# Optimization experiments

Hardware: AMD Instinct MI355X
Metric: run time of the kernel (lower is better)

## Reference

```python
import jax, jax.numpy as jnp
import numpy as np

NUM_HEADS = 16
LAMBDA = 0.1
HADAMARD_SCALE = 0.05
ROPE_BASE = 10000.0


def _rope(t):
    # t: [B, H, S, hd] -- rotary embedding (half-split convention)
    hd = t.shape[-1]
    S = t.shape[2]
    half = hd // 2
    inv_freq = 1.0 / (ROPE_BASE ** (jnp.arange(half, dtype=jnp.float32) / half))
    ang = jnp.arange(S, dtype=jnp.float32)[:, None] * inv_freq[None, :]  # [S, half]
    cos = jnp.cos(ang).astype(t.dtype)
    sin = jnp.sin(ang).astype(t.dtype)
    t1, t2 = t[..., :half], t[..., half:]
    return jnp.concatenate([t1 * cos - t2 * sin, t2 * cos + t1 * sin], axis=-1)


def _rotate_half(t):
    half = t.shape[-1] // 2
    return jnp.concatenate([-t[..., half:], t[..., :half]], axis=-1)


def setup_inputs() -> dict:
    key = jax.random.key(0)
    ks = jax.random.split(key, 6)
    B, S, D = 2, 2048, 1024
    scale = 1.0 / np.sqrt(D).astype(np.float32)
    x = jax.random.normal(ks[0], (B, S, D), jnp.float32)
    Wq = jax.random.normal(ks[1], (D, D), jnp.float32) * scale
    Wk = jax.random.normal(ks[2], (D, D), jnp.float32) * scale
    Wv = jax.random.normal(ks[3], (D, D), jnp.float32) * scale
    Wo = jax.random.normal(ks[4], (D, D), jnp.float32) * scale
    gate_w = jax.random.normal(ks[5], (D // NUM_HEADS,), jnp.float32) * 0.01
    return {"x": x, "Wq": Wq, "Wk": Wk, "Wv": Wv, "Wo": Wo, "gate_w": gate_w}


def reference(x, Wq, Wk, Wv, Wo, gate_w):
    B, S, D = x.shape
    H = NUM_HEADS
    hd = D // H

    def heads(W):
        return (x @ W.T).reshape(B, S, H, hd).transpose(0, 2, 1, 3)  # [B,H,S,hd]

    Q = _rope(heads(Wq))
    K = _rope(heads(Wk))
    V = heads(Wv)

    causal = jnp.tril(jnp.ones((S, S), dtype=bool))
    inv_sqrt_d = 1.0 / jnp.sqrt(jnp.asarray(hd, x.dtype))

    def attend(q, k):
        # first-order + lambda * second-order (elementwise-squared) scores
        s = (jnp.einsum('bhsd,bhtd->bhst', q, k)
             + LAMBDA * jnp.einsum('bhsd,bhtd->bhst', q * q, k * k)) * inv_sqrt_d
        s = jnp.where(causal, s, jnp.asarray(-1e9, s.dtype))
        a = jax.nn.softmax(s, axis=-1)
        return jnp.einsum('bhst,bhtd->bhsd', a, V)

    out1 = attend(Q, K)                                  # standard pass
    out2 = attend(_rotate_half(Q), _rotate_half(K))      # rotated second pass

    # hadamard gate mix of the two passes
    out = 0.5 * (out1 + out2) + HADAMARD_SCALE * (out1 * out2) * gate_w

    out = out.transpose(0, 2, 1, 3).reshape(B, S, D)
    return out @ Wo.T
```

## Files before the change

kernel.cpp:

```cpp
#include <hip/hip_runtime.h>

typedef unsigned short u16;
typedef __attribute__((ext_vector_type(4))) unsigned short u16x4;
typedef __attribute__((ext_vector_type(8))) unsigned short u16x8;
typedef __attribute__((ext_vector_type(8))) short s16x8;
typedef __attribute__((ext_vector_type(4))) float f32x4;

__device__ __forceinline__ u16 f2bf(float f) {
  unsigned int u = __float_as_uint(f);
  u += 0x7FFFu + ((u >> 16) & 1u);
  return (u16)(u >> 16);
}
__device__ __forceinline__ float bf2f(u16 h) {
  return __uint_as_float(((unsigned int)h) << 16);
}

__device__ __forceinline__ void gload_lds16(const u16* g, u16* l) {
  __builtin_amdgcn_global_load_lds(
      (const __attribute__((address_space(1))) unsigned int*)(g),
      (__attribute__((address_space(3))) unsigned int*)(l), 16, 0, 0);
}

__global__ __launch_bounds__(256) void cvt_all(const float* __restrict__ x,
                                               const float* __restrict__ Wq,
                                               const float* __restrict__ Wk,
                                               const float* __restrict__ Wv,
                                               const float* __restrict__ Wo,
                                               u16* __restrict__ xbf,
                                               u16* __restrict__ wbf,
                                               u16* __restrict__ wobf) {
  int blk = blockIdx.x;
  const float* src;
  u16* dst;
  int i;
  if (blk < 4096) {
    src = x; dst = xbf; i = blk * 256 + threadIdx.x;
  } else {
    int wb = blk - 4096;
    int sel = wb >> 10;
    src = (sel == 0) ? Wq : (sel == 1) ? Wk : (sel == 2) ? Wv : Wo;
    dst = (sel < 3) ? (wbf + (size_t)sel * 1048576) : wobf;
    i = (wb & 1023) * 256 + threadIdx.x;
  }
  float4 v = reinterpret_cast<const float4*>(src)[i];
  u16x4 o;
  o.x = f2bf(v.x); o.y = f2bf(v.y); o.z = f2bf(v.z); o.w = f2bf(v.w);
  reinterpret_cast<u16x4*>(dst)[i] = o;
}

__device__ __forceinline__ void store_out(float* p, float v) { *p = v; }
__device__ __forceinline__ void store_out(u16* p, float v) { *p = f2bf(v); }

template <typename OutT, int WM, int WN>
__global__ __launch_bounds__(256) void gemm_bt(const u16* __restrict__ A,
                                               const u16* __restrict__ Bw,
                                               OutT* __restrict__ C, int N, int K) {
  __shared__ u16 As[2][WM * 1024];
  __shared__ u16 Bs[2][WN * 1024];
  const int tid = threadIdx.x;
  const int lane = tid & 63;
  const int wave = tid >> 6;
  const int wm = wave >> 1, wn = wave & 1;
  const int lh = lane & 15, quad = lane >> 4;
  const int q8 = quad * 8;
  const int m0 = blockIdx.y * (WM * 32), n0 = blockIdx.x * (WN * 32);
  constexpr int NCH = 2 * (WM + WN);
  constexpr int PER = NCH / 4;

  auto stage = [&](int buf, int kt) {
    const int kb = kt * 32;
#pragma unroll
    for (int i = 0; i < PER; ++i) {
      const int c = wave * PER + i;
      if (c < 2 * WM) {
        gload_lds16(A + (size_t)(m0 + c * 16 + lh) * K + kb + q8,
                    &As[buf][c * 512 + lane * 8]);
      } else {
        const int rb = c - 2 * WM;
        gload_lds16(Bw + (size_t)(n0 + rb * 16 + lh) * K + kb + q8,
                    &Bs[buf][rb * 512 + lane * 8]);
      }
    }
  };

  f32x4 acc[WM][WN];
#pragma unroll
  for (int i = 0; i < WM; ++i)
#pragma unroll
    for (int j = 0; j < WN; ++j) { acc[i][j][0] = 0.f; acc[i][j][1] = 0.f; acc[i][j][2] = 0.f; acc[i][j][3] = 0.f; }

  const int nkt = K >> 5;
  stage(0, 0);
  __syncthreads();
  for (int kt = 0; kt < nkt; ++kt) {
    const int p = kt & 1;
    if (kt < nkt - 1) stage(1 - p, kt + 1);
    s16x8 af[WM], bf4[WN];
#pragma unroll
    for (int mb = 0; mb < WM; ++mb)
      af[mb] = *reinterpret_cast<const s16x8*>(&As[p][(wm * WM + mb) * 512 + lane * 8]);
#pragma unroll
    for (int nb = 0; nb < WN; ++nb)
      bf4[nb] = *reinterpret_cast<const s16x8*>(&Bs[p][(wn * WN + nb) * 512 + lane * 8]);
#pragma unroll
    for (int mb = 0; mb < WM; ++mb)
#pragma unroll
      for (int nb = 0; nb < WN; ++nb)
        acc[mb][nb] = __builtin_amdgcn_mfma_f32_16x16x32_bf16(af[mb], bf4[nb], acc[mb][nb], 0, 0, 0);
    __syncthreads();
  }
#pragma unroll
  for (int mb = 0; mb < WM; ++mb)
#pragma unroll
    for (int nb = 0; nb < WN; ++nb) {
      const int col = n0 + wn * (WN * 16) + nb * 16 + lh;
#pragma unroll
      for (int r = 0; r < 4; ++r) {
        const int row = m0 + wm * (WM * 16) + mb * 16 + quad * 4 + r;
        store_out(&C[(size_t)row * N + col], acc[mb][nb][r]);
      }
    }
}

__global__ __launch_bounds__(256) void qkv_gemm(const u16* __restrict__ A,
                                                const u16* __restrict__ Bw,
                                                u16* __restrict__ Vt,
                                                u16* __restrict__ Qs,
                                                u16* __restrict__ Kb,
                                                u16* __restrict__ K2b) {
  __shared__ u16 As[2][4096];
  __shared__ u16 Bs[2][4096];
  const int tid = threadIdx.x;
  const int lane = tid & 63;
  const int wave = tid >> 6;
  const int wm = wave >> 1, wn = wave & 1;
  const int lh = lane & 15, quad = lane >> 4;
  const int q8 = quad * 8;
  const int bx = blockIdx.x;
  const int m0 = blockIdx.y * 128, n0 = bx * 128;
  const int K = 1024;

  auto stage = [&](int buf, int kt) {
    const int kb = kt * 32;
#pragma unroll
    for (int i = 0; i < 4; ++i) {
      const int c = wave * 4 + i;
      if (c < 8) {
        gload_lds16(A + (size_t)(m0 + c * 16 + lh) * K + kb + q8,
                    &As[buf][c * 512 + lane * 8]);
      } else {
        const int rb = c - 8;
        gload_lds16(Bw + (size_t)(n0 + rb * 16 + lh) * K + kb + q8,
                    &Bs[buf][rb * 512 + lane * 8]);
      }
    }
  };

  f32x4 acc[4][4];
#pragma unroll
  for (int i = 0; i < 4; ++i)
#pragma unroll
    for (int j = 0; j < 4; ++j) { acc[i][j][0] = 0.f; acc[i][j][1] = 0.f; acc[i][j][2] = 0.f; acc[i][j][3] = 0.f; }

  stage(0, 0);
  __syncthreads();
  for (int kt = 0; kt < 32; ++kt) {
    const int p = kt & 1;
    if (kt < 31) stage(1 - p, kt + 1);
    s16x8 af[4], bf4[4];
#pragma unroll
    for (int mb = 0; mb < 4; ++mb)
      af[mb] = *reinterpret_cast<const s16x8*>(&As[p][(wm * 4 + mb) * 512 + lane * 8]);
#pragma unroll
    for (int nb = 0; nb < 4; ++nb)
      bf4[nb] = *reinterpret_cast<const s16x8*>(&Bs[p][(wn * 4 + nb) * 512 + lane * 8]);
#pragma unroll
    for (int mb = 0; mb < 4; ++mb)
#pragma unroll
      for (int nb = 0; nb < 4; ++nb)
        acc[mb][nb] = __builtin_amdgcn_mfma_f32_16x16x32_bf16(af[mb], bf4[nb], acc[mb][nb], 0, 0, 0);
    __syncthreads();
  }

  if (bx < 16) {
    const bool isQ = (bx < 8);
#pragma unroll
    for (int nb = 0; nb < 2; ++nb) {
      const int d = nb * 16 + lh;
      const float invf = __expf((float)d * -0.2878231366f);
      const int col = n0 + wn * 64 + nb * 16 + lh;
      const int ch = col & 1023;
      const int h = ch >> 6;
#pragma unroll
      for (int mb = 0; mb < 4; ++mb)
#pragma unroll
        for (int r = 0; r < 4; ++r) {
          const int row = m0 + wm * 64 + mb * 16 + quad * 4 + r;
          const int s = row & 2047, b = row >> 11;
          float ang = (float)s * invf;
          float sv, cv;
          __sincosf(ang, &sv, &cv);
          const float v1 = acc[mb][nb][r], v2 = acc[mb][nb + 2][r];
          const float e0 = v1 * cv - v2 * sv;
          const float e1 = v2 * cv + v1 * sv;
          const size_t ofs = (size_t)((b * 16 + h) * 2048 + s) * 64 + d;
          if (isQ) {
            Qs[ofs]      = f2bf(e0 * 0.125f);
            Qs[ofs + 32] = f2bf(e1 * 0.125f);
          } else {
            Kb[ofs]       = f2bf(e0);
            Kb[ofs + 32]  = f2bf(e1);
            K2b[ofs]      = f2bf(e0 * e0);
            K2b[ofs + 32] = f2bf(e1 * e1);
          }
        }
    }
  } else {
#pragma unroll
    for (int mb = 0; mb < 4; ++mb)
#pragma unroll
      for (int nb = 0; nb < 4; ++nb) {
        const int col = n0 + wn * 64 + nb * 16 + lh;
        const int ch = col & 1023;
        const int h = ch >> 6, d = ch & 63;
        const int row0 = m0 + wm * 64 + mb * 16 + quad * 4;
        const int s0 = row0 & 2047, b = row0 >> 11;
        u16x4 o;
#pragma unroll
        for (int r = 0; r < 4; ++r) o[r] = f2bf(acc[mb][nb][r]);
        *reinterpret_cast<u16x4*>(Vt + (size_t)((b * 16 + h) * 64 + d) * 2048 + s0) = o;
      }
  }
}

__global__ __launch_bounds__(256, 2) void attn_kernel(const u16* __restrict__ Qs,
                                                      const u16* __restrict__ Kb,
                                                      const u16* __restrict__ K2b,
                                                      const u16* __restrict__ Vt,
                                                      const float* __restrict__ gate,
                                                      u16* __restrict__ attn,
                                                      float* __restrict__ Opart,
                                                      float* __restrict__ Lpart,
                                                      float* __restrict__ Opart2,
                                                      float* __restrict__ Lpart2) {
  const int lin = blockIdx.y * 44 + blockIdx.x;
  const int xcd = lin & 7;
  const int slot = lin >> 3;
  const int bh = xcd * 4 + (slot / 44);
  const int bxv = slot % 44;

  int qi, kt0, kt1, chunk, which;
  bool split;
  if (bxv < 32) {
    qi = 15 - (bxv >> 2); chunk = bxv & 3; split = true; which = 0;
    const int T = 2 * qi + 2;
    kt0 = (chunk * T) >> 2;
    kt1 = (((chunk + 1) * T) >> 2) - 1;
  } else if (bxv < 40) {
    const int t = bxv - 32;
    qi = 7 - (t >> 1); chunk = t & 1; split = true; which = 1;
    const int nk = qi + 1; kt0 = chunk * nk; kt1 = kt0 + nk - 1;
  } else {
    qi = 43 - bxv; split = false; which = 0; chunk = 0; kt0 = 0; kt1 = 2 * qi + 1;
  }
  const int tid = threadIdx.x, lane = tid & 63, wave = tid >> 6;
  const int lh = lane & 15, quad = lane >> 4;
  const int b = bh >> 4, h = bh & 15;
  __shared__ u16 Pbuf[4][2][1152];
  const int base = qi * 128 + wave * 32;
  const int q8 = quad * 8;

  s16x8 qf[2][2], q2f[2][2];
#pragma unroll
  for (int mb = 0; mb < 2; ++mb) {
    const size_t qoff = (size_t)(bh * 2048 + base + mb * 16 + lh) * 64 + q8;
#pragma unroll
    for (int kk = 0; kk < 2; ++kk) {
      qf[mb][kk] = *reinterpret_cast<const s16x8*>(Qs + qoff + kk * 32);
#pragma unroll
      for (int j = 0; j < 8; ++j) {
        float f = bf2f((u16)qf[mb][kk][j]);
        q2f[mb][kk][j] = (short)f2bf(f * f * 0.8f);
      }
    }
  }

  f32x4 oacc[2][4];
  float lsum[2][4];
#pragma unroll
  for (int mb = 0; mb < 2; ++mb)
#pragma unroll
    for (int nb = 0; nb < 4; ++nb) { oacc[mb][nb][0] = 0.f; oacc[mb][nb][1] = 0.f; oacc[mb][nb][2] = 0.f; oacc[mb][nb][3] = 0.f; }
#pragma unroll
  for (int mb = 0; mb < 2; ++mb)
#pragma unroll
    for (int r = 0; r < 4; ++r) lsum[mb][r] = 0.f;
  float gw[4];
#pragma unroll
  for (int nb = 0; nb < 4; ++nb) gw[nb] = gate[nb * 16 + lh];

  const int wmaxrow = base + 31;
  const int ktdiag = wmaxrow >> 6;
  const int ktw1 = (kt1 < ktdiag) ? kt1 : ktdiag;

  for (int kt = kt0; kt <= ktw1; ++kt) {
    f32x4 sacc[2][4];
#pragma unroll
    for (int mb = 0; mb < 2; ++mb)
#pragma unroll
      for (int nb = 0; nb < 4; ++nb) { sacc[mb][nb][0] = -8.f; sacc[mb][nb][1] = -8.f; sacc[mb][nb][2] = -8.f; sacc[mb][nb][3] = -8.f; }
    __builtin_amdgcn_s_setprio(1);
#pragma unroll
    for (int nb = 0; nb < 4; ++nb) {
      const size_t krow = (size_t)(bh * 2048 + kt * 64 + nb * 16 + lh) * 64 + q8;
#pragma unroll
      for (int kk = 0; kk < 2; ++kk) {
        s16x8 kf  = *reinterpret_cast<const s16x8*>(Kb  + krow + kk * 32);
        s16x8 k2f = *reinterpret_cast<const s16x8*>(K2b + krow + kk * 32);
#pragma unroll
        for (int mb = 0; mb < 2; ++mb) {
          sacc[mb][nb] = __builtin_amdgcn_mfma_f32_16x16x32_bf16(qf[mb][kk],  kf,  sacc[mb][nb], 0, 0, 0);
          sacc[mb][nb] = __builtin_amdgcn_mfma_f32_16x16x32_bf16(q2f[mb][kk], k2f, sacc[mb][nb], 0, 0, 0);
        }
      }
    }
    __builtin_amdgcn_s_setprio(0);
    s16x8 vf[2][4];
#pragma unroll
    for (int kk = 0; kk < 2; ++kk)
#pragma unroll
      for (int nb = 0; nb < 4; ++nb)
        vf[kk][nb] = *reinterpret_cast<const s16x8*>(
            Vt + (size_t)(bh * 64 + nb * 16 + lh) * 2048 + kt * 64 + kk * 32 + q8);

    if (kt * 64 + 63 > base) {
#pragma unroll
      for (int mb = 0; mb < 2; ++mb)
#pragma unroll
        for (int nb = 0; nb < 4; ++nb) {
          const int colg = kt * 64 + nb * 16 + lh;
#pragma unroll
          for (int r = 0; r < 4; ++r) {
            const int rowg = base + mb * 16 + quad * 4 + r;
            if (colg > rowg) sacc[mb][nb][r] = -1e9f;
          }
        }
    }
#pragma unroll
    for (int mb = 0; mb < 2; ++mb)
#pragma unroll
      for (int nb = 0; nb < 4; ++nb)
#pragma unroll
        for (int r = 0; r < 4; ++r) {
          float pv = __expf(sacc[mb][nb][r]);
          lsum[mb][r] += pv;
          Pbuf[wave][mb][(quad * 4 + r) * 72 + nb * 16 + lh] = f2bf(pv);
        }
    __builtin_amdgcn_s_setprio(1);
#pragma unroll
    for (int mb = 0; mb < 2; ++mb)
#pragma unroll
      for (int kk = 0; kk < 2; ++kk) {
        s16x8 pf = *reinterpret_cast<const s16x8*>(&Pbuf[wave][mb][lh * 72 + kk * 32 + q8]);
#pragma unroll
        for (int nb = 0; nb < 4; ++nb)
          oacc[mb][nb] = __builtin_amdgcn_mfma_f32_16x16x32_bf16(pf, vf[kk][nb], oacc[mb][nb], 0, 0, 0);
      }
    __builtin_amdgcn_s_setprio(0);
  }
#pragma unroll
  for (int mb = 0; mb < 2; ++mb)
#pragma unroll
    for (int r = 0; r < 4; ++r) {
      float rs = lsum[mb][r];
#pragma unroll
      for (int off = 1; off < 16; off <<= 1) rs += __shfl_xor(rs, off);
      lsum[mb][r] = rs;
    }
  if (split) {
#pragma unroll
    for (int mb = 0; mb < 2; ++mb)
#pragma unroll
      for (int r = 0; r < 4; ++r) {
        const int rowg = base + mb * 16 + quad * 4 + r;
        if (which == 0) {
          const size_t orow = (size_t)chunk * 32768 + bh * 1024 + (rowg - 1024);
          if (lh == 0) Lpart[orow] = lsum[mb][r];
#pragma unroll
          for (int nb = 0; nb < 4; ++nb)
            Opart[orow * 64 + nb * 16 + lh] = oacc[mb][nb][r];
        } else {
          const size_t orow = (size_t)chunk * 16384 + bh * 512 + (rowg - 512);
          if (lh == 0) Lpart2[orow] = lsum[mb][r];
#pragma unroll
          for (int nb = 0; nb < 4; ++nb)
            Opart2[orow * 64 + nb * 16 + lh] = oacc[mb][nb][r];
        }
      }
  } else {
#pragma unroll
    for (int mb = 0; mb < 2; ++mb)
#pragma unroll
      for (int r = 0; r < 4; ++r) {
        const float invl = 1.0f / lsum[mb][r];
        const int rows = base + mb * 16 + quad * 4 + r;
#pragma unroll
        for (int nb = 0; nb < 4; ++nb) {
          float o = oacc[mb][nb][r] * invl;
          float val = o + 0.05f * o * o * gw[nb];
          attn[(size_t)(b * 2048 + rows) * 1024 + h * 64 + nb * 16 + lh] = f2bf(val);
        }
      }
  }
}

__global__ __launch_bounds__(256) void combine_kernel(const float* __restrict__ Opart,
                                                      const float* __restrict__ Lpart,
                                                      const float* __restrict__ Opart2,
                                                      const float* __restrict__ Lpart2,
                                                      const float* __restrict__ gate,
                                                      u16* __restrict__ attn) {
  int idx = blockIdx.x * 256 + threadIdx.x;
  int d = idx & 63;
  int r_all = idx >> 6;
  float o, l;
  int bh, s;
  if (r_all < 32768) {
    o = Opart[idx] + Opart[idx + 2097152] + Opart[idx + 4194304] + Opart[idx + 6291456];
    l = Lpart[r_all] + Lpart[r_all + 32768] + Lpart[r_all + 65536] + Lpart[r_all + 98304];
    bh = r_all >> 10; s = 1024 + (r_all & 1023);
  } else {
    const int r2 = r_all - 32768;
    const int i2 = idx - 2097152;
    o = Opart2[i2] + Opart2[i2 + 1048576];
    l = Lpart2[r2] + Lpart2[r2 + 16384];
    bh = r2 >> 9; s = 512 + (r2 & 511);
  }
  o /= l;
  float val = o + 0.05f * o * o * gate[d];
  int b = bh >> 4, h = bh & 15;
  attn[(size_t)(b * 2048 + s) * 1024 + h * 64 + d] = f2bf(val);
}

extern "C" void kernel_launch(void* const* d_in, const int* in_sizes, int n_in,
                              void* d_out, int out_size, void* d_ws, size_t ws_size,
                              hipStream_t stream) {
  (void)in_sizes; (void)n_in; (void)out_size; (void)ws_size;
  const float* x    = (const float*)d_in[0];
  const float* Wq   = (const float*)d_in[1];
  const float* Wk   = (const float*)d_in[2];
  const float* Wv   = (const float*)d_in[3];
  const float* Wo   = (const float*)d_in[4];
  const float* gate = (const float*)d_in[5];

  u16* ws    = (u16*)d_ws;
  u16* xbf   = ws;
  u16* wbf   = xbf + 4194304;
  u16* wobf  = wbf + 3145728;
  u16* Qsb   = wobf + 1048576;
  u16* Kbb   = Qsb + 4194304;
  u16* K2bb  = Kbb + 4194304;
  u16* Vtb   = K2bb + 4194304;
  float* Opart  = (float*)(Vtb + 4194304);
  float* Lpart  = Opart + 8388608;
  float* Opart2 = Lpart + 131072;
  float* Lpart2 = Opart2 + 2097152;
  u16* attnb = xbf;

  cvt_all<<<8192, 256, 0, stream>>>(x, Wq, Wk, Wv, Wo, xbf, wbf, wobf);
  qkv_gemm<<<dim3(24, 32), 256, 0, stream>>>(xbf, wbf, Vtb, Qsb, Kbb, K2bb);
  attn_kernel<<<dim3(44, 32), 256, 0, stream>>>(Qsb, Kbb, K2bb, Vtb, gate, attnb,
                                                Opart, Lpart, Opart2, Lpart2);
  combine_kernel<<<12288, 256, 0, stream>>>(Opart, Lpart, Opart2, Lpart2, gate, attnb);
  gemm_bt<float, 4, 2><<<dim3(16, 32), 256, 0, stream>>>(attnb, wobf, (float*)d_out, 1024, 1024);
}
```

Before: 293.8 us.

## Prefetch next K tile into register double buffers during QK MFMAs

The attention loop now splits each K/K² tile load into two halves held in register buffers. The loads for tile kt+1 are issued right after the matching half of tile kt's QK MFMAs, which is meant to hide global load latency behind compute. To make room for the extra 32 live vector registers, launch bounds drop from 2 to 1 block per SM, which lowers occupancy. Base pointers per head are hoisted out of the loop.

```diff
diff --git a/kernel.cpp b/kernel.cpp
--- a/kernel.cpp
+++ b/kernel.cpp
@@ -233,7 +233,22 @@
   }
 }
 
-__global__ __launch_bounds__(256, 2) void attn_kernel(const u16* __restrict__ Qs,
+#define QK_HALF(buf, H)                                                          \
+  _Pragma("unroll")                                                              \
+  for (int i = 0; i < 2; ++i) {                                                  \
+    _Pragma("unroll")                                                            \
+    for (int kk = 0; kk < 2; ++kk) {                                             \
+      _Pragma("unroll")                                                          \
+      for (int mb = 0; mb < 2; ++mb) {                                           \
+        sacc[mb][(H)*2 + i] = __builtin_amdgcn_mfma_f32_16x16x32_bf16(           \
+            qf[mb][kk], buf[(i*2 + kk)*2 + 0], sacc[mb][(H)*2 + i], 0, 0, 0);    \
+        sacc[mb][(H)*2 + i] = __builtin_amdgcn_mfma_f32_16x16x32_bf16(           \
+            q2f[mb][kk], buf[(i*2 + kk)*2 + 1], sacc[mb][(H)*2 + i], 0, 0, 0);   \
+      }                                                                          \
+    }                                                                            \
+  }
+
+__global__ __launch_bounds__(256, 1) void attn_kernel(const u16* __restrict__ Qs,
                                                       const u16* __restrict__ Kb,
                                                       const u16* __restrict__ K2b,
                                                       const u16* __restrict__ Vt,
@@ -270,6 +285,23 @@
   const int base = qi * 128 + wave * 32;
   const int q8 = quad * 8;
 
+  const u16* Kbase  = Kb  + (size_t)bh * 131072;
+  const u16* K2base = K2b + (size_t)bh * 131072;
+  const u16* Vbase  = Vt  + (size_t)bh * 131072;
+
+  auto loadHalf = [&](s16x8 (&buf)[8], int kt, int hh) {
+#pragma unroll
+    for (int i = 0; i < 2; ++i) {
+      const int nb = hh * 2 + i;
+      const size_t krow = (size_t)(kt * 64 + nb * 16 + lh) * 64 + q8;
+#pragma unroll
+      for (int kk = 0; kk < 2; ++kk) {
+        buf[(i * 2 + kk) * 2 + 0] = *reinterpret_cast<const s16x8*>(Kbase + krow + kk * 32);
+        buf[(i * 2 + kk) * 2 + 1] = *reinterpret_cast<const s16x8*>(K2base + krow + kk * 32);
+      }
+    }
+  };
+
   s16x8 qf[2][2], q2f[2][2];
 #pragma unroll
   for (int mb = 0; mb < 2; ++mb) {
@@ -303,35 +335,34 @@
   const int ktdiag = wmaxrow >> 6;
   const int ktw1 = (kt1 < ktdiag) ? kt1 : ktdiag;
 
+  s16x8 bufA[8], bufB[8];
+  loadHalf(bufA, kt0, 0);
+  loadHalf(bufB, kt0, 1);
+
   for (int kt = kt0; kt <= ktw1; ++kt) {
+    const bool more = (kt < ktw1);
     f32x4 sacc[2][4];
 #pragma unroll
     for (int mb = 0; mb < 2; ++mb)
 #pragma unroll
       for (int nb = 0; nb < 4; ++nb) { sacc[mb][nb][0] = -8.f; sacc[mb][nb][1] = -8.f; sacc[mb][nb][2] = -8.f; sacc[mb][nb][3] = -8.f; }
+
     __builtin_amdgcn_s_setprio(1);
-#pragma unroll
-    for (int nb = 0; nb < 4; ++nb) {
-      const size_t krow = (size_t)(bh * 2048 + kt * 64 + nb * 16 + lh) * 64 + q8;
-#pragma unroll
-      for (int kk = 0; kk < 2; ++kk) {
-        s16x8 kf  = *reinterpret_cast<const s16x8*>(Kb  + krow + kk * 32);
-        s16x8 k2f = *reinterpret_cast<const s16x8*>(K2b + krow + kk * 32);
-#pragma unroll
-        for (int mb = 0; mb < 2; ++mb) {
-          sacc[mb][nb] = __builtin_amdgcn_mfma_f32_16x16x32_bf16(qf[mb][kk],  kf,  sacc[mb][nb], 0, 0, 0);
-          sacc[mb][nb] = __builtin_amdgcn_mfma_f32_16x16x32_bf16(q2f[mb][kk], k2f, sacc[mb][nb], 0, 0, 0);
-        }
-      }
-    }
+    QK_HALF(bufA, 0)
     __builtin_amdgcn_s_setprio(0);
+    if (more) loadHalf(bufA, kt + 1, 0);
+    __builtin_amdgcn_s_setprio(1);
+    QK_HALF(bufB, 1)
+    __builtin_amdgcn_s_setprio(0);
+    if (more) loadHalf(bufB, kt + 1, 1);
+
     s16x8 vf[2][4];
 #pragma unroll
     for (int kk = 0; kk < 2; ++kk)
 #pragma unroll
       for (int nb = 0; nb < 4; ++nb)
         vf[kk][nb] = *reinterpret_cast<const s16x8*>(
-            Vt + (size_t)(bh * 64 + nb * 16 + lh) * 2048 + kt * 64 + kk * 32 + q8);
+            Vbase + (size_t)(nb * 16 + lh) * 2048 + kt * 64 + kk * 32 + q8);
 
     if (kt * 64 + 63 > base) {
 #pragma unroll
```

Result: no change. 296.7 us (+1.0%).

## Stage K tiles into LDS with double-buffered async loads over 32-key tiles

Applied to the files above, without the earlier changes.

The attention kernel now uses 32-key tiles instead of 64. K and K-squared tiles are loaded cooperatively into double-buffered shared memory with global_load_lds, and the next tile is prefetched while the current one is computed. Per-wave direct global K loads go away and P buffer use shrinks. The cost is a block-wide __syncthreads every iteration, twice as many loop iterations, and waves idling at the barrier on tiles past their diagonal. The gate weights are now read from global memory at the epilogue rather than kept in registers.

```diff
diff --git a/kernel.cpp b/kernel.cpp
--- a/kernel.cpp
+++ b/kernel.cpp
@@ -253,22 +253,34 @@
   bool split;
   if (bxv < 32) {
     qi = 15 - (bxv >> 2); chunk = bxv & 3; split = true; which = 0;
-    const int T = 2 * qi + 2;
+    const int T = 4 * qi + 4;
     kt0 = (chunk * T) >> 2;
     kt1 = (((chunk + 1) * T) >> 2) - 1;
   } else if (bxv < 40) {
     const int t = bxv - 32;
     qi = 7 - (t >> 1); chunk = t & 1; split = true; which = 1;
-    const int nk = qi + 1; kt0 = chunk * nk; kt1 = kt0 + nk - 1;
+    const int nk = 2 * qi + 2; kt0 = chunk * nk; kt1 = kt0 + nk - 1;
   } else {
-    qi = 43 - bxv; split = false; which = 0; chunk = 0; kt0 = 0; kt1 = 2 * qi + 1;
+    qi = 43 - bxv; split = false; which = 0; chunk = 0; kt0 = 0; kt1 = 4 * qi + 3;
   }
   const int tid = threadIdx.x, lane = tid & 63, wave = tid >> 6;
   const int lh = lane & 15, quad = lane >> 4;
   const int b = bh >> 4, h = bh & 15;
-  __shared__ u16 Pbuf[4][2][1152];
+  __shared__ u16 stageS[2][4096];
+  __shared__ u16 Pbuf[4][640];
   const int base = qi * 128 + wave * 32;
   const int q8 = quad * 8;
+
+  auto do_stage = [&](int buf, int kt) {
+#pragma unroll
+    for (int i = 0; i < 2; ++i) {
+      const int c = wave * 2 + i;
+      const int t2 = c >> 2, f = c & 3, kk = f >> 1, nb = f & 1;
+      const u16* src = (t2 ? K2b : Kb) +
+          (size_t)(bh * 2048 + kt * 32 + nb * 16 + lh) * 64 + kk * 32 + q8;
+      gload_lds16(src, &stageS[buf][t2 * 2048 + f * 512 + lane * 8]);
+    }
+  };
 
   s16x8 qf[2][2], q2f[2][2];
 #pragma unroll
@@ -285,6 +297,8 @@
     }
   }
 
+  const u16* Vbase = Vt + (size_t)bh * 131072;
+
   f32x4 oacc[2][4];
   float lsum[2][4];
 #pragma unroll
@@ -295,78 +309,75 @@
   for (int mb = 0; mb < 2; ++mb)
 #pragma unroll
     for (int r = 0; r < 4; ++r) lsum[mb][r] = 0.f;
-  float gw[4];
-#pragma unroll
-  for (int nb = 0; nb < 4; ++nb) gw[nb] = gate[nb * 16 + lh];
+
+  do_stage(0, kt0);
+  __syncthreads();
 
   const int wmaxrow = base + 31;
-  const int ktdiag = wmaxrow >> 6;
-  const int ktw1 = (kt1 < ktdiag) ? kt1 : ktdiag;
-
-  for (int kt = kt0; kt <= ktw1; ++kt) {
-    f32x4 sacc[2][4];
-#pragma unroll
-    for (int mb = 0; mb < 2; ++mb)
-#pragma unroll
-      for (int nb = 0; nb < 4; ++nb) { sacc[mb][nb][0] = -8.f; sacc[mb][nb][1] = -8.f; sacc[mb][nb][2] = -8.f; sacc[mb][nb][3] = -8.f; }
-    __builtin_amdgcn_s_setprio(1);
-#pragma unroll
-    for (int nb = 0; nb < 4; ++nb) {
-      const size_t krow = (size_t)(bh * 2048 + kt * 64 + nb * 16 + lh) * 64 + q8;
-#pragma unroll
-      for (int kk = 0; kk < 2; ++kk) {
-        s16x8 kf  = *reinterpret_cast<const s16x8*>(Kb  + krow + kk * 32);
-        s16x8 k2f = *reinterpret_cast<const s16x8*>(K2b + krow + kk * 32);
-#pragma unroll
-        for (int mb = 0; mb < 2; ++mb) {
-          sacc[mb][nb] = __builtin_amdgcn_mfma_f32_16x16x32_bf16(qf[mb][kk],  kf,  sacc[mb][nb], 0, 0, 0);
-          sacc[mb][nb] = __builtin_amdgcn_mfma_f32_16x16x32_bf16(q2f[mb][kk], k2f, sacc[mb][nb], 0, 0, 0);
-        }
-      }
-    }
-    __builtin_amdgcn_s_setprio(0);
-    s16x8 vf[2][4];
-#pragma unroll
-    for (int kk = 0; kk < 2; ++kk)
-#pragma unroll
-      for (int nb = 0; nb < 4; ++nb)
-        vf[kk][nb] = *reinterpret_cast<const s16x8*>(
-            Vt + (size_t)(bh * 64 + nb * 16 + lh) * 2048 + kt * 64 + kk * 32 + q8);
-
-    if (kt * 64 + 63 > base) {
+  for (int kt = kt0; kt <= kt1; ++kt) {
+    const int p = (kt - kt0) & 1;
+    if (kt < kt1) do_stage(1 - p, kt + 1);
+
+    if (kt * 32 <= wmaxrow) {
+      const u16* Ks = stageS[p];
+      f32x4 sacc[2][2];
 #pragma unroll
       for (int mb = 0; mb < 2; ++mb)
 #pragma unroll
-        for (int nb = 0; nb < 4; ++nb) {
-          const int colg = kt * 64 + nb * 16 + lh;
-#pragma unroll
-          for (int r = 0; r < 4; ++r) {
-            const int rowg = base + mb * 16 + quad * 4 + r;
-            if (colg > rowg) sacc[mb][nb][r] = -1e9f;
+        for (int nb = 0; nb < 2; ++nb) { sacc[mb][nb][0] = -8.f; sacc[mb][nb][1] = -8.f; sacc[mb][nb][2] = -8.f; sacc[mb][nb][3] = -8.f; }
+      __builtin_amdgcn_s_setprio(1);
+#pragma unroll
+      for (int nb = 0; nb < 2; ++nb)
+#pragma unroll
+        for (int kk = 0; kk < 2; ++kk) {
+          s16x8 kf  = *reinterpret_cast<const s16x8*>(&Ks[(kk * 2 + nb) * 512 + lane * 8]);
+          s16x8 k2f = *reinterpret_cast<const s16x8*>(&Ks[2048 + (kk * 2 + nb) * 512 + lane * 8]);
+#pragma unroll
+          for (int mb = 0; mb < 2; ++mb) {
+            sacc[mb][nb] = __builtin_amdgcn_mfma_f32_16x16x32_bf16(qf[mb][kk],  kf,  sacc[mb][nb], 0, 0, 0);
+            sacc[mb][nb] = __builtin_amdgcn_mfma_f32_16x16x32_bf16(q2f[mb][kk], k2f, sacc[mb][nb], 0, 0, 0);
           }
         }
-    }
-#pragma unroll
-    for (int mb = 0; mb < 2; ++mb)
+      __builtin_amdgcn_s_setprio(0);
+
+      s16x8 vf[4];
 #pragma unroll
       for (int nb = 0; nb < 4; ++nb)
-#pragma unroll
-        for (int r = 0; r < 4; ++r) {
-          float pv = __expf(sacc[mb][nb][r]);
-          lsum[mb][r] += pv;
-          Pbuf[wave][mb][(quad * 4 + r) * 72 + nb * 16 + lh] = f2bf(pv);
-        }
-    __builtin_amdgcn_s_setprio(1);
-#pragma unroll
-    for (int mb = 0; mb < 2; ++mb)
-#pragma unroll
-      for (int kk = 0; kk < 2; ++kk) {
-        s16x8 pf = *reinterpret_cast<const s16x8*>(&Pbuf[wave][mb][lh * 72 + kk * 32 + q8]);
+        vf[nb] = *reinterpret_cast<const s16x8*>(
+            Vbase + (size_t)(nb * 16 + lh) * 2048 + kt * 32 + q8);
+
+      if (kt * 32 + 31 > base) {
+#pragma unroll
+        for (int mb = 0; mb < 2; ++mb)
+#pragma unroll
+          for (int nb = 0; nb < 2; ++nb) {
+            const int colg = kt * 32 + nb * 16 + lh;
+#pragma unroll
+            for (int r = 0; r < 4; ++r) {
+              const int rowg = base + mb * 16 + quad * 4 + r;
+              if (colg > rowg) sacc[mb][nb][r] = -1e9f;
+            }
+          }
+      }
+#pragma unroll
+      for (int mb = 0; mb < 2; ++mb) {
+#pragma unroll
+        for (int nb = 0; nb < 2; ++nb)
+#pragma unroll
+          for (int r = 0; r < 4; ++r) {
+            float pv = __expf(sacc[mb][nb][r]);
+            lsum[mb][r] += pv;
+            Pbuf[wave][(quad * 4 + r) * 40 + nb * 16 + lh] = f2bf(pv);
+          }
+        s16x8 pf = *reinterpret_cast<const s16x8*>(&Pbuf[wave][lh * 40 + q8]);
+        __builtin_amdgcn_s_setprio(1);
 #pragma unroll
         for (int nb = 0; nb < 4; ++nb)
-          oacc[mb][nb] = __builtin_amdgcn_mfma_f32_16x16x32_bf16(pf, vf[kk][nb], oacc[mb][nb], 0, 0, 0);
-      }
-    __builtin_amdgcn_s_setprio(0);
+          oacc[mb][nb] = __builtin_amdgcn_mfma_f32_16x16x32_bf16(pf, vf[nb], oacc[mb][nb], 0, 0, 0);
+        __builtin_amdgcn_s_setprio(0);
+      }
+    }
+    __syncthreads();
   }
 #pragma unroll
   for (int mb = 0; mb < 2; ++mb)
@@ -407,7 +418,7 @@
 #pragma unroll
         for (int nb = 0; nb < 4; ++nb) {
           float o = oacc[mb][nb][r] * invl;
-          float val = o + 0.05f * o * o * gw[nb];
+          float val = o + 0.05f * o * o * gate[nb * 16 + lh];
           attn[(size_t)(b * 2048 + rows) * 1024 + h * 64 + nb * 16 + lh] = f2bf(val);
         }
       }
```

Result: faster. 242.3 us (-17.5%).
